# Kernel tuning notes

Hardware: AMD Instinct MI355X
Metric: run time of the kernel (lower is better)

## Reference

```python
import jax, jax.numpy as jnp
import numpy as np

DIM = 1024

def _circ_conv(x, key):
    # circular convolution along last dim via FFT
    D = x.shape[-1]
    return jnp.fft.irfft(jnp.fft.rfft(x, axis=-1) * jnp.fft.rfft(key), n=D, axis=-1)

def _circ_corr(x, key):
    # circular correlation: conjugate the key spectrum
    D = x.shape[-1]
    return jnp.fft.irfft(jnp.fft.rfft(x, axis=-1) * jnp.conj(jnp.fft.rfft(key)), n=D, axis=-1)

def setup_inputs() -> dict:
    key = jax.random.key(0)
    k0, k1, k2 = jax.random.split(key, 3)
    B, T, D = 4, 2048, DIM
    x = jax.random.normal(k0, (B, T, D), dtype=jnp.float32)
    bind_key = jax.random.normal(k1, (D,), dtype=jnp.float32) * 0.02
    unbind_key = jax.random.normal(k2, (D,), dtype=jnp.float32) * 0.02
    gate = jnp.ones((1,), dtype=jnp.float32)
    decay = jnp.asarray(0.9, dtype=jnp.float32)
    return {"x": x, "bind_key": bind_key, "unbind_key": unbind_key, "gate": gate, "decay": decay}

def reference(x, bind_key, unbind_key, gate, decay):
    B, T, D = x.shape
    bound = _circ_conv(x, bind_key)                      # (B, T, D)
    d = jax.nn.sigmoid(decay)
    pos = jnp.arange(T, dtype=x.dtype)
    diff = pos[:, None] - pos[None, :]                   # (T, T)
    causal = diff >= 0
    # clamp exponent to avoid inf*0 on masked (t < s) entries; math identical to tril mask
    decay_matrix = jnp.where(causal, d ** jnp.maximum(diff, 0.0), 0.0)
    hologram = jnp.einsum('ts,bsd->btd', decay_matrix, bound)
    retrieved = _circ_corr(hologram, unbind_key)
    return x + gate * retrieved
```

## Files before the change

### kernel.cpp

```cpp
#include <hip/hip_runtime.h>
#include <hip/hip_bf16.h>

constexpr int Dd = 1024;
constexpr int Tt = 2048;
constexpr int Bb = 4;
constexpr int Rr = Bb * Tt;
constexpr int RSN = 1032;
constexpr int BM  = 64;
constexpr int BN  = 128;
constexpr int BK  = 64;
constexpr int NST = Dd / BK;
constexpr int NPAN = Rr / BM;

typedef __attribute__((ext_vector_type(2))) float f32x2;
typedef __attribute__((ext_vector_type(16))) float f32x16;
typedef __attribute__((ext_vector_type(8))) short bf16x8;

__device__ __forceinline__ float sigmoidf_(float v) {
    return 1.0f / (1.0f + expf(-v));
}

__global__ void k_c(const float* __restrict__ bind,
                    const float* __restrict__ unbind,
                    const float* __restrict__ x,
                    const float* __restrict__ decay,
                    float* __restrict__ c,
                    float* __restrict__ Sw) {
    const int tid = threadIdx.x;
    if (blockIdx.x < 64) {
        __shared__ float sb[Dd];
        __shared__ float su[Dd];
        __shared__ float sp[256];
        for (int j = tid; j < Dd; j += 256) { sb[j] = bind[j]; su[j] = unbind[j]; }
        __syncthreads();
        const int n_loc = tid >> 4;
        const int seg = tid & 15;
        const int n = (int)blockIdx.x * 16 + n_loc;
        float acc = 0.f;
        #pragma unroll 8
        for (int i = 0; i < 64; ++i) {
            const int m = i * 16 + seg;
            acc = fmaf(su[m], sb[(m + n) & (Dd - 1)], acc);
        }
        sp[tid] = acc;
        __syncthreads();
        if (tid < 16) {
            float s = 0.f;
            #pragma unroll
            for (int j = 0; j < 16; ++j) s += sp[tid * 16 + j];
            c[(int)blockIdx.x * 16 + tid] = s;
        }
    } else {
        const int w = (int)blockIdx.x - 64;
        const int p = (w >> 1) + 1;
        const int h = w & 1;
        const float dd = sigmoidf_(decay[0]);
        const int col = h * 512 + tid * 2;
        const float* xp = x + (size_t)(p * BM - 32) * Dd + col;
        f32x2 s8 = (f32x2){0.f, 0.f}, s9 = (f32x2){0.f, 0.f};
        #pragma unroll
        for (int i = 0; i < 16; ++i)
            s8 = dd * s8 + *(const f32x2*)&xp[(size_t)i * Dd];
        #pragma unroll
        for (int i = 16; i < 32; ++i)
            s9 = dd * s9 + *(const f32x2*)&xp[(size_t)i * Dd];
        *(f32x2*)&Sw[((size_t)p * 2 + 0) * Dd + col] = s8;
        *(f32x2*)&Sw[((size_t)p * 2 + 1) * Dd + col] = s9;
    }
}

__global__ __launch_bounds__(128, 2) void k_fused(
    const float* __restrict__ x,
    const float* __restrict__ c,
    const float* __restrict__ Sw,
    const float* __restrict__ decay,
    const float* __restrict__ gate,
    float* __restrict__ out)
{
    __shared__ __align__(16) __hip_bfloat16 sA[2][BM * BK];
    __shared__ __align__(16) __hip_bfloat16 rs[8][RSN];
    __shared__ float sS[6][BK];

    const int tid = threadIdx.x;
    const int wave = tid >> 6;
    const int lane = tid & 63;

    const int id  = blockIdx.x;
    const int xcd = id & 7;
    const int rr  = id >> 3;
    const int in_ = rr & 7;
    const int gg  = rr >> 3;
    const int im  = xcd * 16 + gg;
    const int tile_m = im * BM;
    const int tile_n = in_ * BN;
    const int pw  = im & 31;

    const int phase = ((in_ & 1) << 3) | ((gg & 1) << 2);
#define P(T) (((T) + phase) & 15)

    const float dd = sigmoidf_(decay[0]);
    const float d2 = dd * dd, d4 = d2 * d2, d8 = d4 * d4;
    const float d16 = d8 * d8, d32 = d16 * d16;

    #pragma unroll
    for (int s = 0; s < 8; ++s)
        for (int t = tid; t < RSN; t += 128)
            rs[s][t] = __float2bfloat16(c[(-(t + s)) & (Dd - 1)]);

    const int cp = tid & 31;
    const int s  = tid >> 5;
    const bool wldz = (pw == 0);

    f32x2 vmA[16], vmB[16];
    f32x2 swA = (f32x2){0.f, 0.f}, swB = (f32x2){0.f, 0.f};

#define LOADSTRIP(V, SWR, ST) do {                                          \
    const int col_ = (ST) * BK + 2 * cp;                                    \
    const float* xp_ = x + (size_t)(tile_m + s * 16) * Dd + col_;           \
    _Pragma("unroll")                                                       \
    for (int i_ = 0; i_ < 16; ++i_)                                         \
        V[i_] = *(const f32x2*)&xp_[(size_t)i_ * Dd];                       \
    if (s >= 2 && !wldz)                                                    \
        SWR = *(const f32x2*)&Sw[((size_t)im * 2 + (s - 2)) * Dd + col_];   \
} while (0)

#define CHAINS(V, SWR) do {                                                 \
    _Pragma("unroll")                                                       \
    for (int i_ = 1; i_ < 16; ++i_) V[i_] = dd * V[i_ - 1] + V[i_];         \
    *(f32x2*)&sS[s][2 * cp] = V[15];                                        \
    if (s >= 2)                                                             \
        *(f32x2*)&sS[4 + (s - 2)][2 * cp] =                                 \
            wldz ? (f32x2){0.f, 0.f} : SWR;                                 \
} while (0)

    auto loadS = [&](int r) -> f32x2 {
        if (r >= 0)  return *(const f32x2*)&sS[r][2 * cp];
        if (r == -1) return *(const f32x2*)&sS[5][2 * cp];
        if (r == -2) return *(const f32x2*)&sS[4][2 * cp];
        return (f32x2){0.f, 0.f};
    };

#define FINISH(V, BB) do {                                                  \
    f32x2 C_ = loadS(s - 1) + d16 * loadS(s - 2) + d32 * loadS(s - 3);      \
    float w_ = dd;                                                          \
    _Pragma("unroll")                                                       \
    for (int i_ = 0; i_ < 16; ++i_) {                                       \
        f32x2 h_ = V[i_] + w_ * C_;                                         \
        w_ *= dd;                                                           \
        const int rl_ = s * 16 + i_;                                        \
        const int pos_ = (((2 * cp) >> 3) ^ (rl_ & 7)) * 8 + ((2 * cp) & 7);\
        union { __hip_bfloat16 b; unsigned short u; } ux_, uy_;             \
        ux_.b = __float2bfloat16(h_[0]);                                    \
        uy_.b = __float2bfloat16(h_[1]);                                    \
        ushort2 o_; o_.x = ux_.u; o_.y = uy_.u;                             \
        *(ushort2*)&sA[BB][rl_ * 64 + pos_] = o_;                           \
    }                                                                       \
} while (0)

    const int wn  = wave * 64;
    const int fm  = lane & 31;
    const int fsw = fm & 7;
    const int fc0 = lane >> 5;
    const int ng0 = tile_n + wn + fm;

    f32x16 acc[2][2];
    #pragma unroll
    for (int i = 0; i < 2; ++i)
        #pragma unroll
        for (int j = 0; j < 2; ++j)
            #pragma unroll
            for (int e = 0; e < 16; ++e)
                acc[i][j][e] = 0.f;

#define MF(BB, K0) do {                                                     \
    _Pragma("unroll")                                                       \
    for (int kh_ = 0; kh_ < 4; ++kh_) {                                     \
        const int kc_ = kh_ * 2 + fc0;                                      \
        const int ck_ = (K0) + kc_ * 8;                                     \
        bf16x8 af0_ = *(const bf16x8*)                                      \
            &sA[BB][(fm) * 64 + (kc_ ^ fsw) * 8];                           \
        bf16x8 af1_ = *(const bf16x8*)                                      \
            &sA[BB][(32 + fm) * 64 + (kc_ ^ fsw) * 8];                      \
        const int bi0_ = (ck_ - ng0) & (Dd - 1);                            \
        const int bi1_ = (ck_ - ng0 - 32) & (Dd - 1);                       \
        bf16x8 bf0_ = *(const bf16x8*)&rs[bi0_ & 7][bi0_ & ~7];             \
        bf16x8 bf1_ = *(const bf16x8*)&rs[bi1_ & 7][bi1_ & ~7];             \
        acc[0][0] = __builtin_amdgcn_mfma_f32_32x32x16_bf16(                \
            af0_, bf0_, acc[0][0], 0, 0, 0);                                \
        acc[0][1] = __builtin_amdgcn_mfma_f32_32x32x16_bf16(                \
            af0_, bf1_, acc[0][1], 0, 0, 0);                                \
        acc[1][0] = __builtin_amdgcn_mfma_f32_32x32x16_bf16(                \
            af1_, bf0_, acc[1][0], 0, 0, 0);                                \
        acc[1][1] = __builtin_amdgcn_mfma_f32_32x32x16_bf16(                \
            af1_, bf1_, acc[1][1], 0, 0, 0);                                \
    }                                                                       \
} while (0)

    LOADSTRIP(vmA, swA, P(0));
    LOADSTRIP(vmB, swB, P(1));
    CHAINS(vmA, swA);
    __syncthreads();
    FINISH(vmA, 0);
    __syncthreads();

    for (int st = 0; st < NST; st += 2) {
        if (st + 2 < NST) LOADSTRIP(vmA, swA, P(st + 2));
        MF(0, P(st) * BK);
        CHAINS(vmB, swB);
        __syncthreads();
        FINISH(vmB, 1);
        __syncthreads();
        if (st + 3 < NST) LOADSTRIP(vmB, swB, P(st + 3));
        MF(1, P(st + 1) * BK);
        if (st + 2 < NST) {
            CHAINS(vmA, swA);
            __syncthreads();
            FINISH(vmA, 0);
        }
        __syncthreads();
    }

#undef LOADSTRIP
#undef CHAINS
#undef FINISH
#undef MF
#undef P

    const float g = gate[0];
    #pragma unroll
    for (int sm = 0; sm < 2; ++sm) {
        #pragma unroll
        for (int sn = 0; sn < 2; ++sn) {
            const int colg = tile_n + wn + sn * 32 + (lane & 31);
            #pragma unroll
            for (int g1 = 0; g1 < 4; ++g1) {
                const int row0 = tile_m + sm * 32 + g1 * 8 + (lane >> 5) * 4;
                #pragma unroll
                for (int r0 = 0; r0 < 4; ++r0) {
                    const size_t off = (size_t)(row0 + r0) * Dd + colg;
                    out[off] = fmaf(g, acc[sm][sn][g1 * 4 + r0], x[off]);
                }
            }
        }
    }
}

extern "C" void kernel_launch(void* const* d_in, const int* in_sizes, int n_in,
                              void* d_out, int out_size, void* d_ws, size_t ws_size,
                              hipStream_t stream) {
    const float* x      = (const float*)d_in[0];
    const float* bind   = (const float*)d_in[1];
    const float* unbind = (const float*)d_in[2];
    const float* gate   = (const float*)d_in[3];
    const float* decay  = (const float*)d_in[4];
    float* out = (float*)d_out;

    float* c  = (float*)d_ws;
    float* Sw = (float*)((char*)d_ws + 4096);

    k_c    <<<dim3(64 + 2 * (NPAN - 1)), dim3(256), 0, stream>>>(
        bind, unbind, x, decay, c, Sw);
    k_fused<<<dim3(1024), dim3(128), 0, stream>>>(x, c, Sw, decay, gate, out);
}
```

Measured before the change: 125.8 us.

## Double fused kernel threads to 256 with 8-row decay strips and 32-column waves

Raises the fused kernel block from 128 to 256 threads (4 waves). Each thread now scans 8 rows instead of 16, and each wave computes a 64x32 output slice instead of 64x64. The pre-pass now writes four 8-row chunk sums per panel, and the carry combine uses four prior strip sums (powers d8, d16, d24). The aim is more parallelism and more waves per CU to hide the serial decay scan and load latency. In exchange, each wave does half the MFMAs per A-fragment load and there is more combine and shared-memory traffic.

New measurement: 156.9 us. 24.7% more time.

```diff
diff --git a/kernel.cpp b/kernel.cpp
--- a/kernel.cpp
+++ b/kernel.cpp
@@ -57,19 +57,18 @@
         const float dd = sigmoidf_(decay[0]);
         const int col = h * 512 + tid * 2;
         const float* xp = x + (size_t)(p * BM - 32) * Dd + col;
-        f32x2 s8 = (f32x2){0.f, 0.f}, s9 = (f32x2){0.f, 0.f};
         #pragma unroll
-        for (int i = 0; i < 16; ++i)
-            s8 = dd * s8 + *(const f32x2*)&xp[(size_t)i * Dd];
-        #pragma unroll
-        for (int i = 16; i < 32; ++i)
-            s9 = dd * s9 + *(const f32x2*)&xp[(size_t)i * Dd];
-        *(f32x2*)&Sw[((size_t)p * 2 + 0) * Dd + col] = s8;
-        *(f32x2*)&Sw[((size_t)p * 2 + 1) * Dd + col] = s9;
+        for (int j = 0; j < 4; ++j) {
+            f32x2 sj = (f32x2){0.f, 0.f};
+            #pragma unroll
+            for (int i = 0; i < 8; ++i)
+                sj = dd * sj + *(const f32x2*)&xp[(size_t)(j * 8 + i) * Dd];
+            *(f32x2*)&Sw[((size_t)p * 4 + j) * Dd + col] = sj;
+        }
     }
 }
 
-__global__ __launch_bounds__(128, 2) void k_fused(
+__global__ __launch_bounds__(256, 4) void k_fused(
     const float* __restrict__ x,
     const float* __restrict__ c,
     const float* __restrict__ Sw,
@@ -79,7 +78,7 @@
 {
     __shared__ __align__(16) __hip_bfloat16 sA[2][BM * BK];
     __shared__ __align__(16) __hip_bfloat16 rs[8][RSN];
-    __shared__ float sS[6][BK];
+    __shared__ float sS[12][BK];
 
     const int tid = threadIdx.x;
     const int wave = tid >> 6;
@@ -100,54 +99,53 @@
 
     const float dd = sigmoidf_(decay[0]);
     const float d2 = dd * dd, d4 = d2 * d2, d8 = d4 * d4;
-    const float d16 = d8 * d8, d32 = d16 * d16;
+    const float d16 = d8 * d8, d24 = d16 * d8;
 
     #pragma unroll
     for (int s = 0; s < 8; ++s)
-        for (int t = tid; t < RSN; t += 128)
+        for (int t = tid; t < RSN; t += 256)
             rs[s][t] = __float2bfloat16(c[(-(t + s)) & (Dd - 1)]);
 
     const int cp = tid & 31;
     const int s  = tid >> 5;
     const bool wldz = (pw == 0);
 
-    f32x2 vmA[16], vmB[16];
+    f32x2 vmA[8], vmB[8];
     f32x2 swA = (f32x2){0.f, 0.f}, swB = (f32x2){0.f, 0.f};
 
 #define LOADSTRIP(V, SWR, ST) do {                                          \
     const int col_ = (ST) * BK + 2 * cp;                                    \
-    const float* xp_ = x + (size_t)(tile_m + s * 16) * Dd + col_;           \
-    _Pragma("unroll")                                                       \
-    for (int i_ = 0; i_ < 16; ++i_)                                         \
+    const float* xp_ = x + (size_t)(tile_m + s * 8) * Dd + col_;            \
+    _Pragma("unroll")                                                       \
+    for (int i_ = 0; i_ < 8; ++i_)                                          \
         V[i_] = *(const f32x2*)&xp_[(size_t)i_ * Dd];                       \
-    if (s >= 2 && !wldz)                                                    \
-        SWR = *(const f32x2*)&Sw[((size_t)im * 2 + (s - 2)) * Dd + col_];   \
+    if (s >= 4 && !wldz)                                                    \
+        SWR = *(const f32x2*)&Sw[((size_t)im * 4 + (s - 4)) * Dd + col_];   \
 } while (0)
 
 #define CHAINS(V, SWR) do {                                                 \
     _Pragma("unroll")                                                       \
-    for (int i_ = 1; i_ < 16; ++i_) V[i_] = dd * V[i_ - 1] + V[i_];         \
-    *(f32x2*)&sS[s][2 * cp] = V[15];                                        \
-    if (s >= 2)                                                             \
-        *(f32x2*)&sS[4 + (s - 2)][2 * cp] =                                 \
+    for (int i_ = 1; i_ < 8; ++i_) V[i_] = dd * V[i_ - 1] + V[i_];          \
+    *(f32x2*)&sS[s][2 * cp] = V[7];                                         \
+    if (s >= 4)                                                             \
+        *(f32x2*)&sS[8 + (s - 4)][2 * cp] =                                 \
             wldz ? (f32x2){0.f, 0.f} : SWR;                                 \
 } while (0)
 
     auto loadS = [&](int r) -> f32x2 {
-        if (r >= 0)  return *(const f32x2*)&sS[r][2 * cp];
-        if (r == -1) return *(const f32x2*)&sS[5][2 * cp];
-        if (r == -2) return *(const f32x2*)&sS[4][2 * cp];
-        return (f32x2){0.f, 0.f};
+        if (r >= 0) return *(const f32x2*)&sS[r][2 * cp];
+        return *(const f32x2*)&sS[12 + r][2 * cp];
     };
 
 #define FINISH(V, BB) do {                                                  \
-    f32x2 C_ = loadS(s - 1) + d16 * loadS(s - 2) + d32 * loadS(s - 3);      \
+    f32x2 C_ = loadS(s - 1) + d8 * loadS(s - 2)                             \
+             + d16 * loadS(s - 3) + d24 * loadS(s - 4);                     \
     float w_ = dd;                                                          \
     _Pragma("unroll")                                                       \
-    for (int i_ = 0; i_ < 16; ++i_) {                                       \
+    for (int i_ = 0; i_ < 8; ++i_) {                                        \
         f32x2 h_ = V[i_] + w_ * C_;                                         \
         w_ *= dd;                                                           \
-        const int rl_ = s * 16 + i_;                                        \
+        const int rl_ = s * 8 + i_;                                         \
         const int pos_ = (((2 * cp) >> 3) ^ (rl_ & 7)) * 8 + ((2 * cp) & 7);\
         union { __hip_bfloat16 b; unsigned short u; } ux_, uy_;             \
         ux_.b = __float2bfloat16(h_[0]);                                    \
@@ -157,20 +155,18 @@
     }                                                                       \
 } while (0)
 
-    const int wn  = wave * 64;
+    const int wn  = wave * 32;
     const int fm  = lane & 31;
     const int fsw = fm & 7;
     const int fc0 = lane >> 5;
     const int ng0 = tile_n + wn + fm;
 
-    f32x16 acc[2][2];
+    f32x16 acc[2];
     #pragma unroll
     for (int i = 0; i < 2; ++i)
         #pragma unroll
-        for (int j = 0; j < 2; ++j)
-            #pragma unroll
-            for (int e = 0; e < 16; ++e)
-                acc[i][j][e] = 0.f;
+        for (int e = 0; e < 16; ++e)
+            acc[i][e] = 0.f;
 
 #define MF(BB, K0) do {                                                     \
     _Pragma("unroll")                                                       \
@@ -182,17 +178,11 @@
         bf16x8 af1_ = *(const bf16x8*)                                      \
             &sA[BB][(32 + fm) * 64 + (kc_ ^ fsw) * 8];                      \
         const int bi0_ = (ck_ - ng0) & (Dd - 1);                            \
-        const int bi1_ = (ck_ - ng0 - 32) & (Dd - 1);                       \
         bf16x8 bf0_ = *(const bf16x8*)&rs[bi0_ & 7][bi0_ & ~7];             \
-        bf16x8 bf1_ = *(const bf16x8*)&rs[bi1_ & 7][bi1_ & ~7];             \
-        acc[0][0] = __builtin_amdgcn_mfma_f32_32x32x16_bf16(                \
-            af0_, bf0_, acc[0][0], 0, 0, 0);                                \
-        acc[0][1] = __builtin_amdgcn_mfma_f32_32x32x16_bf16(                \
-            af0_, bf1_, acc[0][1], 0, 0, 0);                                \
-        acc[1][0] = __builtin_amdgcn_mfma_f32_32x32x16_bf16(                \
-            af1_, bf0_, acc[1][0], 0, 0, 0);                                \
-        acc[1][1] = __builtin_amdgcn_mfma_f32_32x32x16_bf16(                \
-            af1_, bf1_, acc[1][1], 0, 0, 0);                                \
+        acc[0] = __builtin_amdgcn_mfma_f32_32x32x16_bf16(                   \
+            af0_, bf0_, acc[0], 0, 0, 0);                                   \
+        acc[1] = __builtin_amdgcn_mfma_f32_32x32x16_bf16(                   \
+            af1_, bf0_, acc[1], 0, 0, 0);                                   \
     }                                                                       \
 } while (0)
 
@@ -227,19 +217,16 @@
 #undef P
 
     const float g = gate[0];
+    const int colg = tile_n + wn + (lane & 31);
     #pragma unroll
     for (int sm = 0; sm < 2; ++sm) {
         #pragma unroll
-        for (int sn = 0; sn < 2; ++sn) {
-            const int colg = tile_n + wn + sn * 32 + (lane & 31);
+        for (int g1 = 0; g1 < 4; ++g1) {
+            const int row0 = tile_m + sm * 32 + g1 * 8 + (lane >> 5) * 4;
             #pragma unroll
-            for (int g1 = 0; g1 < 4; ++g1) {
-                const int row0 = tile_m + sm * 32 + g1 * 8 + (lane >> 5) * 4;
-                #pragma unroll
-                for (int r0 = 0; r0 < 4; ++r0) {
-                    const size_t off = (size_t)(row0 + r0) * Dd + colg;
-                    out[off] = fmaf(g, acc[sm][sn][g1 * 4 + r0], x[off]);
-                }
+            for (int r0 = 0; r0 < 4; ++r0) {
+                const size_t off = (size_t)(row0 + r0) * Dd + colg;
+                out[off] = fmaf(g, acc[sm][g1 * 4 + r0], x[off]);
             }
         }
     }
@@ -260,5 +247,5 @@
 
     k_c    <<<dim3(64 + 2 * (NPAN - 1)), dim3(256), 0, stream>>>(
         bind, unbind, x, decay, c, Sw);
-    k_fused<<<dim3(1024), dim3(128), 0, stream>>>(x, c, Sw, decay, gate, out);
-}
+    k_fused<<<dim3(1024), dim3(256), 0, stream>>>(x, c, Sw, decay, gate, out);
+}
```
